# Kernel tuning notes

Hardware: AMD Instinct MI355X
Metric: run time of the kernel (lower is better)

## Reference

```python
import jax, jax.numpy as jnp
import numpy as np

B, N, D, H, DD = 4, 256, 768, 12, 64
HD = D // H  # head_dim = 64
SCALE = float(np.sqrt(HD))


def _layernorm(x, g, b, eps=1e-5):
    mu = jnp.mean(x, axis=-1, keepdims=True)
    var = jnp.var(x, axis=-1, keepdims=True)
    return (x - mu) / jnp.sqrt(var + eps) * g + b


def setup_inputs() -> dict:
    key = jax.random.key(0)
    ks = jax.random.split(key, 20)
    def w(k, shape, fan_in):
        return (jax.random.normal(k, shape, jnp.float32) / np.sqrt(fan_in)).astype(jnp.float32)
    x = jax.random.normal(ks[0], (B, N, D), jnp.float32)
    dist = jax.random.normal(ks[1], (B, N, N, DD), jnp.float32)
    mask = jax.random.randint(ks[2], (B, N, N), 0, 2) > 0
    eye = jnp.eye(N, dtype=bool)[None]
    edge_mask = jnp.logical_or(mask, eye)  # guarantee no fully-masked row
    return {
        'x': x, 'distance_features': dist, 'edge_mask': edge_mask,
        'qkv_w': w(ks[3], (D, 3 * D), D), 'qkv_b': jnp.zeros((3 * D,), jnp.float32),
        'out_w': w(ks[4], (D, D), D), 'out_b': jnp.zeros((D,), jnp.float32),
        'rb_w1': w(ks[5], (DD, D), DD), 'rb_b1': jnp.zeros((D,), jnp.float32),
        'rb_w2': w(ks[6], (D, H), D), 'rb_b2': jnp.zeros((H,), jnp.float32),
        'gate_w1': w(ks[7], (D, D), D), 'gate_b1': jnp.zeros((D,), jnp.float32),
        'gate_w2': w(ks[8], (D, D), D), 'gate_b2': jnp.zeros((D,), jnp.float32),
        'ff_w1': w(ks[9], (D, 2 * D), D), 'ff_b1': jnp.zeros((2 * D,), jnp.float32),
        'ff_w2': w(ks[10], (2 * D, D), 2 * D), 'ff_b2': jnp.zeros((D,), jnp.float32),
        'ln1_g': jnp.ones((D,), jnp.float32), 'ln1_b': jnp.zeros((D,), jnp.float32),
        'ln2_g': jnp.ones((D,), jnp.float32), 'ln2_b': jnp.zeros((D,), jnp.float32),
    }


def reference(x, distance_features, edge_mask, qkv_w, qkv_b, out_w, out_b,
              rb_w1, rb_b1, rb_w2, rb_b2, gate_w1, gate_b1, gate_w2, gate_b2,
              ff_w1, ff_b1, ff_w2, ff_b2, ln1_g, ln1_b, ln2_g, ln2_b):
    residual = x
    xn = _layernorm(x, ln1_g, ln1_b)
    qkv = xn @ qkv_w + qkv_b
    q, k, v = jnp.split(qkv, 3, axis=-1)
    q = q.reshape(B, N, H, HD)
    k = k.reshape(B, N, H, HD)
    v = v.reshape(B, N, H, HD)
    logits = jnp.einsum('bihd,bjhd->bhij', q, k) / SCALE
    bias = jax.nn.silu(distance_features @ rb_w1 + rb_b1) @ rb_w2 + rb_b2  # [B,N,N,H]
    logits = logits + jnp.transpose(bias, (0, 3, 1, 2))
    neg = jnp.finfo(logits.dtype).min
    logits = jnp.where(edge_mask[:, None, :, :], logits, neg)
    attn = jax.nn.softmax(logits, axis=-1)
    context = jnp.einsum('bhij,bjhd->bihd', attn, v).reshape(B, N, D)
    gated = jax.nn.silu(xn @ gate_w1 + gate_b1) @ gate_w2 + gate_b2
    x2 = residual + (context * jax.nn.sigmoid(gated)) @ out_w + out_b
    y = _layernorm(x2, ln2_g, ln2_b)
    ff = jax.nn.gelu(y @ ff_w1 + ff_b1, approximate=False) @ ff_w2 + ff_b2
    return x2 + ff
```

## Files before the change

### kernel.cpp

```cpp
#include <hip/hip_runtime.h>
#include <cmath>

#define U16 unsigned short

typedef __bf16 bf16x8_t __attribute__((ext_vector_type(8)));
typedef float f32x4_t __attribute__((ext_vector_type(4)));

union Frag { uint4 u4; unsigned u[4]; bf16x8_t b8; U16 s[8]; };

__device__ __forceinline__ float b2f(U16 u) {
  union { unsigned int i; float f; } x; x.i = ((unsigned int)u) << 16; return x.f;
}
__device__ __forceinline__ U16 f2b(float f) {
  union { float f; unsigned int i; } x; x.f = f;
  unsigned int r = x.i + 0x7FFFu + ((x.i >> 16) & 1u);
  return (U16)(r >> 16);
}
__device__ __forceinline__ unsigned pack2bf_fast(float a, float b) {
  union { float f; unsigned u; } xa, xb; xa.f = a; xb.f = b;
  return __builtin_amdgcn_perm(xb.u + 0x8000u, xa.u + 0x8000u, 0x07060302);
}
__device__ __forceinline__ float fast_silu(float z) {
  return z * __builtin_amdgcn_rcpf(1.f + __expf(-z));
}

__global__ __launch_bounds__(256) void prep_kernel(
    const float* __restrict__ qkv_w, const float* __restrict__ out_w,
    const float* __restrict__ g1w, const float* __restrict__ g2w,
    const float* __restrict__ ff1w, const float* __restrict__ ff2w,
    const float* __restrict__ rb1w, const float* __restrict__ rb2w,
    U16* __restrict__ qkv_wT, U16* __restrict__ out_wT, U16* __restrict__ g1wT,
    U16* __restrict__ g2wT, U16* __restrict__ ff1wT, U16* __restrict__ ff2wT,
    U16* __restrict__ rb1wT, U16* __restrict__ rb2wL) {
  int bid = blockIdx.x;
  if (bid >= 5808) {
    int idx = (bid - 5808) * 256 + threadIdx.x;
    int j = idx & 7, lane = (idx >> 3) & 63, pp = idx >> 9;
    int row = lane & 15, col = pp * 32 + ((lane >> 4) << 3) + j;
    rb2wL[idx] = (row < 12) ? f2b(rb2w[col * 12 + row]) : (U16)0;
    return;
  }
  const float* in; U16* out; int R, C, base;
  if (bid < 1728)      { in = qkv_w; out = qkv_wT; R = 768;  C = 2304; base = 0; }
  else if (bid < 2304) { in = out_w; out = out_wT; R = 768;  C = 768;  base = 1728; }
  else if (bid < 2880) { in = g1w;   out = g1wT;   R = 768;  C = 768;  base = 2304; }
  else if (bid < 3456) { in = g2w;   out = g2wT;   R = 768;  C = 768;  base = 2880; }
  else if (bid < 4608) { in = ff1w;  out = ff1wT;  R = 768;  C = 1536; base = 3456; }
  else if (bid < 5760) { in = ff2w;  out = ff2wT;  R = 1536; C = 768;  base = 4608; }
  else                 { in = rb1w;  out = rb1wT;  R = 64;   C = 768;  base = 5760; }
  int bx = bid - base, tilesx = C / 32;
  int c0 = (bx % tilesx) * 32, r0 = (bx / tilesx) * 32;
  __shared__ float tile[32][33];
  int tx = threadIdx.x & 31, ty = threadIdx.x >> 5;
#pragma unroll
  for (int yy = 0; yy < 4; ++yy)
    tile[ty + yy * 8][tx] = in[(size_t)(r0 + ty + yy * 8) * C + c0 + tx];
  __syncthreads();
#pragma unroll
  for (int yy = 0; yy < 4; ++yy)
    out[(size_t)(c0 + ty + yy * 8) * R + r0 + tx] = f2b(tile[tx][ty + yy * 8]);
}

__global__ __launch_bounds__(256) void ln_kernel(const float* __restrict__ X,
                                                 const float* __restrict__ gam,
                                                 const float* __restrict__ bet,
                                                 U16* __restrict__ Y) {
  int row = blockIdx.x, tid = threadIdx.x;
  __shared__ float r1[256], r2[256];
  float v[3];
#pragma unroll
  for (int j = 0; j < 3; ++j) v[j] = X[(size_t)row * 768 + tid + j * 256];
  r1[tid] = v[0] + v[1] + v[2];
  r2[tid] = v[0] * v[0] + v[1] * v[1] + v[2] * v[2];
  __syncthreads();
  for (int s = 128; s > 0; s >>= 1) {
    if (tid < s) { r1[tid] += r1[tid + s]; r2[tid] += r2[tid + s]; }
    __syncthreads();
  }
  float mean = r1[0] * (1.f / 768.f);
  float var = r2[0] * (1.f / 768.f) - mean * mean;
  float rstd = rsqrtf(var + 1e-5f);
#pragma unroll
  for (int j = 0; j < 3; ++j) {
    int c = tid + j * 256;
    Y[(size_t)row * 768 + c] = f2b((v[j] - mean) * rstd * gam[c] + bet[c]);
  }
}

#define LDP 40
template <int EPI, bool OUTF32>
__global__ __launch_bounds__(256) void gemm_bt(const U16* __restrict__ A,
                                               const U16* __restrict__ BT,
                                               const float* __restrict__ bias,
                                               const float* __restrict__ other,
                                               void* __restrict__ Cout,
                                               int M, int N, int K) {
  __shared__ __align__(16) U16 sA[64 * LDP];
  __shared__ __align__(16) U16 sB[64 * LDP];
  int tid = threadIdx.x;
  int lane = tid & 63, wave = tid >> 6;
  int m0 = blockIdx.y * 64, n0 = blockIdx.x * 64;
  int wm = (wave >> 1) * 32, wn = (wave & 1) * 32;
  int lm = lane & 15, lq = lane >> 4;
  int srow = tid >> 2;
  int scol = (tid & 3) * 8;
  f32x4_t acc[2][2] = {};
  for (int k0 = 0; k0 < K; k0 += 32) {
    __syncthreads();
    uint4 a0 = *(const uint4*)(A + (size_t)(m0 + srow) * K + k0 + scol);
    uint4 b0 = *(const uint4*)(BT + (size_t)(n0 + srow) * K + k0 + scol);
    *(uint4*)&sA[srow * LDP + scol] = a0;
    *(uint4*)&sB[srow * LDP + scol] = b0;
    __syncthreads();
    Frag af[2], bf[2];
#pragma unroll
    for (int mt = 0; mt < 2; ++mt)
      af[mt].u4 = *(const uint4*)&sA[(wm + mt * 16 + lm) * LDP + lq * 8];
#pragma unroll
    for (int nt = 0; nt < 2; ++nt)
      bf[nt].u4 = *(const uint4*)&sB[(wn + nt * 16 + lm) * LDP + lq * 8];
#pragma unroll
    for (int mt = 0; mt < 2; ++mt)
#pragma unroll
      for (int nt = 0; nt < 2; ++nt)
        acc[mt][nt] = __builtin_amdgcn_mfma_f32_16x16x32_bf16(af[mt].b8, bf[nt].b8,
                                                              acc[mt][nt], 0, 0, 0);
  }
#pragma unroll
  for (int nt = 0; nt < 2; ++nt) {
    int gc = n0 + wn + nt * 16 + lm;
    float bz = bias[gc];
#pragma unroll
    for (int mt = 0; mt < 2; ++mt) {
#pragma unroll
      for (int r = 0; r < 4; ++r) {
        int gr = m0 + wm + mt * 16 + lq * 4 + r;
        size_t idx = (size_t)gr * N + gc;
        float z = acc[mt][nt][r] + bz;
        float o;
        if (EPI == 0) o = z;
        else if (EPI == 1) o = fast_silu(z);
        else if (EPI == 2) o = 0.5f * z * (1.f + erff(z * 0.70710678118f));
        else if (EPI == 3) o = other[idx] * __builtin_amdgcn_rcpf(1.f + __expf(-z));
        else o = z + other[idx];
        if (OUTF32) ((float*)Cout)[idx] = o;
        else ((U16*)Cout)[idx] = f2b(o);
      }
    }
  }
}

__global__ __launch_bounds__(256) void rb_kernel(const float* __restrict__ dist,
                                                 const U16* __restrict__ w1T,
                                                 const float* __restrict__ b1,
                                                 const U16* __restrict__ w2L,
                                                 const float* __restrict__ b2,
                                                 float* __restrict__ biasOut) {
  int tid = threadIdx.x;
  int lane = tid & 63, wave = tid >> 6;
  int lm = lane & 15, lq = lane >> 4;
  int r0 = blockIdx.x * 256;
  Frag bd[4][2];
#pragma unroll
  for (int g = 0; g < 4; ++g) {
    const float* ap = dist + (size_t)(r0 + (wave * 4 + g) * 16 + lm) * 64 + lq * 8;
    float4 v0 = ((const float4*)ap)[0];
    float4 v1 = ((const float4*)ap)[1];
    float4 v2 = ((const float4*)(ap + 32))[0];
    float4 v3 = ((const float4*)(ap + 32))[1];
    bd[g][0].u[0] = pack2bf_fast(v0.x, v0.y); bd[g][0].u[1] = pack2bf_fast(v0.z, v0.w);
    bd[g][0].u[2] = pack2bf_fast(v1.x, v1.y); bd[g][0].u[3] = pack2bf_fast(v1.z, v1.w);
    bd[g][1].u[0] = pack2bf_fast(v2.x, v2.y); bd[g][1].u[1] = pack2bf_fast(v2.z, v2.w);
    bd[g][1].u[2] = pack2bf_fast(v3.x, v3.y); bd[g][1].u[3] = pack2bf_fast(v3.z, v3.w);
  }
  const U16* w1p0 = w1T + (size_t)(((lm >> 2) << 3) + (lm & 3)) * 64 + lq * 8;
  const U16* w1p1 = w1p0 + 4 * 64;
  const U16* w2p = w2L + lane * 8;
  const float* b1p = b1 + lq * 8;
  f32x4_t bacc[4] = {};
  for (int pp = 0; pp < 24; ++pp) {
    Frag w00, w01, w10, w11, wb;
    w00.u4 = *(const uint4*)w1p0;
    w01.u4 = *(const uint4*)(w1p0 + 32);
    w10.u4 = *(const uint4*)w1p1;
    w11.u4 = *(const uint4*)(w1p1 + 32);
    wb.u4 = *(const uint4*)w2p;
    float4 bb0 = *(const float4*)b1p;
    float4 bb1 = *(const float4*)(b1p + 4);
#pragma unroll
    for (int g = 0; g < 4; ++g) {
      f32x4_t z0 = {0.f, 0.f, 0.f, 0.f}, z1 = {0.f, 0.f, 0.f, 0.f};
      z0 = __builtin_amdgcn_mfma_f32_16x16x32_bf16(w00.b8, bd[g][0].b8, z0, 0, 0, 0);
      z0 = __builtin_amdgcn_mfma_f32_16x16x32_bf16(w01.b8, bd[g][1].b8, z0, 0, 0, 0);
      z1 = __builtin_amdgcn_mfma_f32_16x16x32_bf16(w10.b8, bd[g][0].b8, z1, 0, 0, 0);
      z1 = __builtin_amdgcn_mfma_f32_16x16x32_bf16(w11.b8, bd[g][1].b8, z1, 0, 0, 0);
      float s0 = fast_silu(z0[0] + bb0.x), s1 = fast_silu(z0[1] + bb0.y);
      float s2 = fast_silu(z0[2] + bb0.z), s3 = fast_silu(z0[3] + bb0.w);
      float t0 = fast_silu(z1[0] + bb1.x), t1 = fast_silu(z1[1] + bb1.y);
      float t2 = fast_silu(z1[2] + bb1.z), t3 = fast_silu(z1[3] + bb1.w);
      Frag af2;
      af2.u[0] = pack2bf_fast(s0, s1); af2.u[1] = pack2bf_fast(s2, s3);
      af2.u[2] = pack2bf_fast(t0, t1); af2.u[3] = pack2bf_fast(t2, t3);
      bacc[g] = __builtin_amdgcn_mfma_f32_16x16x32_bf16(af2.b8, wb.b8, bacc[g], 0, 0, 0);
    }
    w1p0 += 32 * 64; w1p1 += 32 * 64; w2p += 64 * 8; b1p += 32;
  }
  int h = lm;
  if (h < 12) {
    float hb = b2[h];
#pragma unroll
    for (int g = 0; g < 4; ++g) {
#pragma unroll
      for (int r = 0; r < 4; ++r) {
        int gr = r0 + (wave * 4 + g) * 16 + lq * 4 + r;
        int b = gr >> 16, rem = gr & 65535, i = rem >> 8, j = rem & 255;
        biasOut[(((size_t)b * 12 + h) * 256 + i) * 256 + j] = bacc[g][r] + hb;
      }
    }
  }
}

__global__ __launch_bounds__(256) void attn_kernel(const float* __restrict__ qkv,
                                                   const float* __restrict__ biasB,
                                                   const int* __restrict__ mask,
                                                   float* __restrict__ ctx) {
  int tid = threadIdx.x, lane = tid & 63, w = tid >> 6;
  int bh = blockIdx.y, b = bh / 12, h = bh % 12;
  int i0 = blockIdx.x * 16;
  __shared__ float sQ[16][68];
  __shared__ float sP[4][4][256];
  {
    int r = tid >> 4, c = (tid & 15) * 4;
    *(float4*)&sQ[r][c] = *(const float4*)&qkv[((size_t)(b * 256 + i0 + r)) * 2304 + h * 64 + c];
  }
  __syncthreads();
  int iw = i0 + w * 4;
  float lacc[4][4] = {};
  const float* kbase = qkv + (size_t)b * 256 * 2304 + 768 + h * 64 + (size_t)lane * 2304;
#pragma unroll 4
  for (int dc = 0; dc < 16; ++dc) {
    float4 k0 = *(const float4*)(kbase + (size_t)0 * 64 * 2304 + dc * 4);
    float4 k1 = *(const float4*)(kbase + (size_t)1 * 64 * 2304 + dc * 4);
    float4 k2 = *(const float4*)(kbase + (size_t)2 * 64 * 2304 + dc * 4);
    float4 k3 = *(const float4*)(kbase + (size_t)3 * 64 * 2304 + dc * 4);
#pragma unroll
    for (int qi = 0; qi < 4; ++qi) {
      float4 q4 = *(const float4*)&sQ[w * 4 + qi][dc * 4];
      lacc[qi][0] += q4.x * k0.x + q4.y * k0.y + q4.z * k0.z + q4.w * k0.w;
      lacc[qi][1] += q4.x * k1.x + q4.y * k1.y + q4.z * k1.z + q4.w * k1.w;
      lacc[qi][2] += q4.x * k2.x + q4.y * k2.y + q4.z * k2.z + q4.w * k2.w;
      lacc[qi][3] += q4.x * k3.x + q4.y * k3.y + q4.z * k3.z + q4.w * k3.w;
    }
  }
#pragma unroll
  for (int qi = 0; qi < 4; ++qi) {
    int gi = iw + qi;
    const float* brow = biasB + (((size_t)b * 12 + h) * 256 + gi) * 256;
    const int* mrow = mask + ((size_t)b * 256 + gi) * 256;
    float lg[4];
#pragma unroll
    for (int jc = 0; jc < 4; ++jc) {
      float lv = lacc[qi][jc] * 0.125f + brow[jc * 64 + lane];
      lg[jc] = mrow[jc * 64 + lane] ? lv : -1e30f;
    }
    float mx = fmaxf(fmaxf(lg[0], lg[1]), fmaxf(lg[2], lg[3]));
#pragma unroll
    for (int m = 32; m > 0; m >>= 1) mx = fmaxf(mx, __shfl_xor(mx, m));
    float e[4], sum = 0.f;
#pragma unroll
    for (int jc = 0; jc < 4; ++jc) { e[jc] = __expf(lg[jc] - mx); sum += e[jc]; }
#pragma unroll
    for (int m = 32; m > 0; m >>= 1) sum += __shfl_xor(sum, m);
    float inv = __builtin_amdgcn_rcpf(sum);
#pragma unroll
    for (int jc = 0; jc < 4; ++jc) sP[w][qi][jc * 64 + lane] = e[jc] * inv;
  }
  __syncthreads();
  float ca[4] = {0.f, 0.f, 0.f, 0.f};
  const float* vcol = qkv + (size_t)b * 256 * 2304 + 1536 + h * 64 + lane;
#pragma unroll 2
  for (int j4 = 0; j4 < 256; j4 += 4) {
    float4 p0 = *(const float4*)&sP[w][0][j4];
    float4 p1 = *(const float4*)&sP[w][1][j4];
    float4 p2 = *(const float4*)&sP[w][2][j4];
    float4 p3 = *(const float4*)&sP[w][3][j4];
    const float* pp0 = (const float*)&p0;
    const float* pp1 = (const float*)&p1;
    const float* pp2 = (const float*)&p2;
    const float* pp3 = (const float*)&p3;
#pragma unroll
    for (int jj = 0; jj < 4; ++jj) {
      float v = vcol[(size_t)(j4 + jj) * 2304];
      ca[0] += pp0[jj] * v;
      ca[1] += pp1[jj] * v;
      ca[2] += pp2[jj] * v;
      ca[3] += pp3[jj] * v;
    }
  }
#pragma unroll
  for (int qi = 0; qi < 4; ++qi)
    ctx[((size_t)(b * 256 + iw + qi)) * 768 + h * 64 + lane] = ca[qi];
}

extern "C" void kernel_launch(void* const* d_in, const int* in_sizes, int n_in,
                              void* d_out, int out_size, void* d_ws, size_t ws_size,
                              hipStream_t stream) {
  const float* x       = (const float*)d_in[0];
  const float* dist    = (const float*)d_in[1];
  const int* mask      = (const int*)d_in[2];
  const float* qkv_w   = (const float*)d_in[3];
  const float* qkv_b   = (const float*)d_in[4];
  const float* out_w   = (const float*)d_in[5];
  const float* out_b   = (const float*)d_in[6];
  const float* rb_w1   = (const float*)d_in[7];
  const float* rb_b1   = (const float*)d_in[8];
  const float* rb_w2   = (const float*)d_in[9];
  const float* rb_b2   = (const float*)d_in[10];
  const float* gate_w1 = (const float*)d_in[11];
  const float* gate_b1 = (const float*)d_in[12];
  const float* gate_w2 = (const float*)d_in[13];
  const float* gate_b2 = (const float*)d_in[14];
  const float* ff_w1   = (const float*)d_in[15];
  const float* ff_b1   = (const float*)d_in[16];
  const float* ff_w2   = (const float*)d_in[17];
  const float* ff_b2   = (const float*)d_in[18];
  const float* ln1_g   = (const float*)d_in[19];
  const float* ln1_b   = (const float*)d_in[20];
  const float* ln2_g   = (const float*)d_in[21];
  const float* ln2_b   = (const float*)d_in[22];

  char* w = (char*)d_ws;
  auto alloc = [&](size_t bytes) {
    char* p = w;
    w += (bytes + 255) & ~(size_t)255;
    return p;
  };
  U16* xn      = (U16*)alloc(1024 * 768 * 2);
  float* qkvb  = (float*)alloc((size_t)1024 * 2304 * 4);
  U16* qkv_wT  = (U16*)alloc(2304 * 768 * 2);
  U16* out_wT  = (U16*)alloc(768 * 768 * 2);
  U16* g1wT    = (U16*)alloc(768 * 768 * 2);
  U16* g2wT    = (U16*)alloc(768 * 768 * 2);
  U16* ff1wT   = (U16*)alloc(1536 * 768 * 2);
  U16* ff2wT   = (U16*)alloc(768 * 1536 * 2);
  U16* rb1wT   = (U16*)alloc(768 * 64 * 2);
  U16* rb2wL   = (U16*)alloc(24 * 64 * 8 * 2);
  float* biasB = (float*)alloc((size_t)4 * 12 * 256 * 256 * 4);
  float* ctx   = (float*)alloc(1024 * 768 * 4);
  U16* g1      = (U16*)alloc(1024 * 768 * 2);
  U16* cg      = (U16*)alloc(1024 * 768 * 2);
  float* x2    = (float*)alloc(1024 * 768 * 4);
  U16* y       = (U16*)alloc(1024 * 768 * 2);
  U16* f1      = (U16*)alloc(1024 * 1536 * 2);
  (void)ws_size; (void)in_sizes; (void)n_in; (void)out_size;

  prep_kernel<<<5856, 256, 0, stream>>>(qkv_w, out_w, gate_w1, gate_w2, ff_w1, ff_w2,
                                        rb_w1, rb_w2, qkv_wT, out_wT, g1wT, g2wT,
                                        ff1wT, ff2wT, rb1wT, rb2wL);

  ln_kernel<<<1024, 256, 0, stream>>>(x, ln1_g, ln1_b, xn);
  gemm_bt<0, true><<<dim3(36, 16), 256, 0, stream>>>(xn, qkv_wT, qkv_b, nullptr, qkvb,
                                                     1024, 2304, 768);
  rb_kernel<<<1024, 256, 0, stream>>>(dist, rb1wT, rb_b1, rb2wL, rb_b2, biasB);
  attn_kernel<<<dim3(16, 48), 256, 0, stream>>>(qkvb, biasB, mask, ctx);
  gemm_bt<1, false><<<dim3(12, 16), 256, 0, stream>>>(xn, g1wT, gate_b1, nullptr, g1,
                                                      1024, 768, 768);
  gemm_bt<3, false><<<dim3(12, 16), 256, 0, stream>>>(g1, g2wT, gate_b2, ctx, cg,
                                                      1024, 768, 768);
  gemm_bt<4, true><<<dim3(12, 16), 256, 0, stream>>>(cg, out_wT, out_b, x, x2,
                                                     1024, 768, 768);
  ln_kernel<<<1024, 256, 0, stream>>>(x2, ln2_g, ln2_b, y);
  gemm_bt<2, false><<<dim3(24, 16), 256, 0, stream>>>(y, ff1wT, ff_b1, nullptr, f1,
                                                      1024, 1536, 768);
  gemm_bt<4, true><<<dim3(12, 16), 256, 0, stream>>>(f1, ff2wT, ff_b2, x2, (float*)d_out,
                                                     1024, 768, 1536);
}
```

Baseline: 369.6 us.

## Pre-transpose K for coalesced attention loads and fold biases into MFMA accumulators

Adds a kernel that transposes the K slice of the QKV output into a per-head [d][n] layout. The attention logits loop can then read K with lane-contiguous, coalesced loads instead of per-lane rows strided by 2304 floats. The attention kernel also drops two __syncthreads that only guarded wave-private shared data. In the relative-bias kernel, both biases are seeded as MFMA accumulator initial values rather than added afterwards, and bf16 packing uses the hardware packed-convert intrinsic. The cost is an extra launch plus a write and re-read of a 3 MB K buffer.

```diff
diff --git a/kernel.cpp b/kernel.cpp
--- a/kernel.cpp
+++ b/kernel.cpp
@@ -1,4 +1,5 @@
 #include <hip/hip_runtime.h>
+#include <hip/hip_bf16.h>
 #include <cmath>
 
 #define U16 unsigned short
@@ -15,6 +16,11 @@
   union { float f; unsigned int i; } x; x.f = f;
   unsigned int r = x.i + 0x7FFFu + ((x.i >> 16) & 1u);
   return (U16)(r >> 16);
+}
+__device__ __forceinline__ unsigned cvt_pk_bf16(float a, float b) {
+  union { __hip_bfloat162 h2; unsigned u; } x;
+  x.h2 = __float22bfloat162_rn(make_float2(a, b));
+  return x.u;
 }
 __device__ __forceinline__ unsigned pack2bf_fast(float a, float b) {
   union { float f; unsigned u; } xa, xb; xa.f = a; xb.f = b;
@@ -59,6 +65,24 @@
 #pragma unroll
   for (int yy = 0; yy < 4; ++yy)
     out[(size_t)(c0 + ty + yy * 8) * R + r0 + tx] = f2b(tile[tx][ty + yy * 8]);
+}
+
+__global__ __launch_bounds__(256) void kt_kernel(const float* __restrict__ qkvb,
+                                                 float* __restrict__ kT) {
+  int bid = blockIdx.x;
+  int bh = bid >> 4, tile = bid & 15;
+  int b = bh / 12, h = bh % 12;
+  int n0 = (tile & 7) * 32, d0 = (tile >> 3) * 32;
+  __shared__ float t[32][33];
+  int tx = threadIdx.x & 31, ty = threadIdx.x >> 5;
+#pragma unroll
+  for (int yy = 0; yy < 4; ++yy)
+    t[ty + yy * 8][tx] =
+        qkvb[(size_t)(b * 256 + n0 + ty + yy * 8) * 2304 + 768 + h * 64 + d0 + tx];
+  __syncthreads();
+#pragma unroll
+  for (int yy = 0; yy < 4; ++yy)
+    kT[(size_t)bh * 16384 + (size_t)(d0 + ty + yy * 8) * 256 + n0 + tx] = t[tx][ty + yy * 8];
 }
 
 __global__ __launch_bounds__(256) void ln_kernel(const float* __restrict__ X,
@@ -160,6 +184,7 @@
   int lane = tid & 63, wave = tid >> 6;
   int lm = lane & 15, lq = lane >> 4;
   int r0 = blockIdx.x * 256;
+  float hb = (lm < 12) ? b2[lm] : 0.f;
   Frag bd[4][2];
 #pragma unroll
   for (int g = 0; g < 4; ++g) {
@@ -168,16 +193,16 @@
     float4 v1 = ((const float4*)ap)[1];
     float4 v2 = ((const float4*)(ap + 32))[0];
     float4 v3 = ((const float4*)(ap + 32))[1];
-    bd[g][0].u[0] = pack2bf_fast(v0.x, v0.y); bd[g][0].u[1] = pack2bf_fast(v0.z, v0.w);
-    bd[g][0].u[2] = pack2bf_fast(v1.x, v1.y); bd[g][0].u[3] = pack2bf_fast(v1.z, v1.w);
-    bd[g][1].u[0] = pack2bf_fast(v2.x, v2.y); bd[g][1].u[1] = pack2bf_fast(v2.z, v2.w);
-    bd[g][1].u[2] = pack2bf_fast(v3.x, v3.y); bd[g][1].u[3] = pack2bf_fast(v3.z, v3.w);
+    bd[g][0].u[0] = cvt_pk_bf16(v0.x, v0.y); bd[g][0].u[1] = cvt_pk_bf16(v0.z, v0.w);
+    bd[g][0].u[2] = cvt_pk_bf16(v1.x, v1.y); bd[g][0].u[3] = cvt_pk_bf16(v1.z, v1.w);
+    bd[g][1].u[0] = cvt_pk_bf16(v2.x, v2.y); bd[g][1].u[1] = cvt_pk_bf16(v2.z, v2.w);
+    bd[g][1].u[2] = cvt_pk_bf16(v3.x, v3.y); bd[g][1].u[3] = cvt_pk_bf16(v3.z, v3.w);
   }
   const U16* w1p0 = w1T + (size_t)(((lm >> 2) << 3) + (lm & 3)) * 64 + lq * 8;
   const U16* w1p1 = w1p0 + 4 * 64;
   const U16* w2p = w2L + lane * 8;
   const float* b1p = b1 + lq * 8;
-  f32x4_t bacc[4] = {};
+  f32x4_t bacc[4] = {{hb, hb, hb, hb}, {hb, hb, hb, hb}, {hb, hb, hb, hb}, {hb, hb, hb, hb}};
   for (int pp = 0; pp < 24; ++pp) {
     Frag w00, w01, w10, w11, wb;
     w00.u4 = *(const uint4*)w1p0;
@@ -187,69 +212,70 @@
     wb.u4 = *(const uint4*)w2p;
     float4 bb0 = *(const float4*)b1p;
     float4 bb1 = *(const float4*)(b1p + 4);
+    f32x4_t cz0 = {bb0.x, bb0.y, bb0.z, bb0.w};
+    f32x4_t cz1 = {bb1.x, bb1.y, bb1.z, bb1.w};
 #pragma unroll
     for (int g = 0; g < 4; ++g) {
-      f32x4_t z0 = {0.f, 0.f, 0.f, 0.f}, z1 = {0.f, 0.f, 0.f, 0.f};
+      f32x4_t z0 = cz0, z1 = cz1;
       z0 = __builtin_amdgcn_mfma_f32_16x16x32_bf16(w00.b8, bd[g][0].b8, z0, 0, 0, 0);
       z0 = __builtin_amdgcn_mfma_f32_16x16x32_bf16(w01.b8, bd[g][1].b8, z0, 0, 0, 0);
       z1 = __builtin_amdgcn_mfma_f32_16x16x32_bf16(w10.b8, bd[g][0].b8, z1, 0, 0, 0);
       z1 = __builtin_amdgcn_mfma_f32_16x16x32_bf16(w11.b8, bd[g][1].b8, z1, 0, 0, 0);
-      float s0 = fast_silu(z0[0] + bb0.x), s1 = fast_silu(z0[1] + bb0.y);
-      float s2 = fast_silu(z0[2] + bb0.z), s3 = fast_silu(z0[3] + bb0.w);
-      float t0 = fast_silu(z1[0] + bb1.x), t1 = fast_silu(z1[1] + bb1.y);
-      float t2 = fast_silu(z1[2] + bb1.z), t3 = fast_silu(z1[3] + bb1.w);
+      float s0 = fast_silu(z0[0]), s1 = fast_silu(z0[1]);
+      float s2 = fast_silu(z0[2]), s3 = fast_silu(z0[3]);
+      float t0 = fast_silu(z1[0]), t1 = fast_silu(z1[1]);
+      float t2 = fast_silu(z1[2]), t3 = fast_silu(z1[3]);
       Frag af2;
-      af2.u[0] = pack2bf_fast(s0, s1); af2.u[1] = pack2bf_fast(s2, s3);
-      af2.u[2] = pack2bf_fast(t0, t1); af2.u[3] = pack2bf_fast(t2, t3);
+      af2.u[0] = cvt_pk_bf16(s0, s1); af2.u[1] = cvt_pk_bf16(s2, s3);
+      af2.u[2] = cvt_pk_bf16(t0, t1); af2.u[3] = cvt_pk_bf16(t2, t3);
       bacc[g] = __builtin_amdgcn_mfma_f32_16x16x32_bf16(af2.b8, wb.b8, bacc[g], 0, 0, 0);
     }
     w1p0 += 32 * 64; w1p1 += 32 * 64; w2p += 64 * 8; b1p += 32;
   }
-  int h = lm;
-  if (h < 12) {
-    float hb = b2[h];
+  if (lm < 12) {
 #pragma unroll
     for (int g = 0; g < 4; ++g) {
 #pragma unroll
       for (int r = 0; r < 4; ++r) {
         int gr = r0 + (wave * 4 + g) * 16 + lq * 4 + r;
         int b = gr >> 16, rem = gr & 65535, i = rem >> 8, j = rem & 255;
-        biasOut[(((size_t)b * 12 + h) * 256 + i) * 256 + j] = bacc[g][r] + hb;
+        biasOut[(((size_t)b * 12 + lm) * 256 + i) * 256 + j] = bacc[g][r];
       }
     }
   }
 }
 
 __global__ __launch_bounds__(256) void attn_kernel(const float* __restrict__ qkv,
+                                                   const float* __restrict__ kT,
                                                    const float* __restrict__ biasB,
                                                    const int* __restrict__ mask,
                                                    float* __restrict__ ctx) {
   int tid = threadIdx.x, lane = tid & 63, w = tid >> 6;
   int bh = blockIdx.y, b = bh / 12, h = bh % 12;
   int i0 = blockIdx.x * 16;
-  __shared__ float sQ[16][68];
+  __shared__ float sQ[16][66];
   __shared__ float sP[4][4][256];
   {
     int r = tid >> 4, c = (tid & 15) * 4;
-    *(float4*)&sQ[r][c] = *(const float4*)&qkv[((size_t)(b * 256 + i0 + r)) * 2304 + h * 64 + c];
-  }
-  __syncthreads();
+    *(float4*)&sQ[r][c] =
+        *(const float4*)&qkv[((size_t)(b * 256 + i0 + r)) * 2304 + h * 64 + c];
+  }
   int iw = i0 + w * 4;
   float lacc[4][4] = {};
-  const float* kbase = qkv + (size_t)b * 256 * 2304 + 768 + h * 64 + (size_t)lane * 2304;
+  const float* kp = kT + (size_t)bh * 16384 + lane;
 #pragma unroll 4
-  for (int dc = 0; dc < 16; ++dc) {
-    float4 k0 = *(const float4*)(kbase + (size_t)0 * 64 * 2304 + dc * 4);
-    float4 k1 = *(const float4*)(kbase + (size_t)1 * 64 * 2304 + dc * 4);
-    float4 k2 = *(const float4*)(kbase + (size_t)2 * 64 * 2304 + dc * 4);
-    float4 k3 = *(const float4*)(kbase + (size_t)3 * 64 * 2304 + dc * 4);
+  for (int d = 0; d < 64; d += 2) {
+    float k00 = kp[d * 256], k01 = kp[d * 256 + 64];
+    float k02 = kp[d * 256 + 128], k03 = kp[d * 256 + 192];
+    float k10 = kp[d * 256 + 256], k11 = kp[d * 256 + 320];
+    float k12 = kp[d * 256 + 384], k13 = kp[d * 256 + 448];
 #pragma unroll
     for (int qi = 0; qi < 4; ++qi) {
-      float4 q4 = *(const float4*)&sQ[w * 4 + qi][dc * 4];
-      lacc[qi][0] += q4.x * k0.x + q4.y * k0.y + q4.z * k0.z + q4.w * k0.w;
-      lacc[qi][1] += q4.x * k1.x + q4.y * k1.y + q4.z * k1.z + q4.w * k1.w;
-      lacc[qi][2] += q4.x * k2.x + q4.y * k2.y + q4.z * k2.z + q4.w * k2.w;
-      lacc[qi][3] += q4.x * k3.x + q4.y * k3.y + q4.z * k3.z + q4.w * k3.w;
+      float2 q2 = *(const float2*)&sQ[w * 4 + qi][d];
+      lacc[qi][0] += q2.x * k00 + q2.y * k10;
+      lacc[qi][1] += q2.x * k01 + q2.y * k11;
+      lacc[qi][2] += q2.x * k02 + q2.y * k12;
+      lacc[qi][3] += q2.x * k03 + q2.y * k13;
     }
   }
 #pragma unroll
@@ -275,7 +301,6 @@
 #pragma unroll
     for (int jc = 0; jc < 4; ++jc) sP[w][qi][jc * 64 + lane] = e[jc] * inv;
   }
-  __syncthreads();
   float ca[4] = {0.f, 0.f, 0.f, 0.f};
   const float* vcol = qkv + (size_t)b * 256 * 2304 + 1536 + h * 64 + lane;
 #pragma unroll 2
@@ -337,6 +362,7 @@
   };
   U16* xn      = (U16*)alloc(1024 * 768 * 2);
   float* qkvb  = (float*)alloc((size_t)1024 * 2304 * 4);
+  float* kT    = (float*)alloc((size_t)48 * 64 * 256 * 4);
   U16* qkv_wT  = (U16*)alloc(2304 * 768 * 2);
   U16* out_wT  = (U16*)alloc(768 * 768 * 2);
   U16* g1wT    = (U16*)alloc(768 * 768 * 2);
@@ -361,8 +387,9 @@
   ln_kernel<<<1024, 256, 0, stream>>>(x, ln1_g, ln1_b, xn);
   gemm_bt<0, true><<<dim3(36, 16), 256, 0, stream>>>(xn, qkv_wT, qkv_b, nullptr, qkvb,
                                                      1024, 2304, 768);
+  kt_kernel<<<768, 256, 0, stream>>>(qkvb, kT);
   rb_kernel<<<1024, 256, 0, stream>>>(dist, rb1wT, rb_b1, rb2wL, rb_b2, biasB);
-  attn_kernel<<<dim3(16, 48), 256, 0, stream>>>(qkvb, biasB, mask, ctx);
+  attn_kernel<<<dim3(16, 48), 256, 0, stream>>>(qkvb, kT, biasB, mask, ctx);
   gemm_bt<1, false><<<dim3(12, 16), 256, 0, stream>>>(xn, g1wT, gate_b1, nullptr, g1,
                                                       1024, 768, 768);
   gemm_bt<3, false><<<dim3(12, 16), 256, 0, stream>>>(g1, g2wT, gate_b2, ctx, cg,
```

New measurement: 353.8 us. 4.3% less time.
